# Kernel tuning notes

Measured on AMD Instinct MI355X. Metric: run time of the kernel, lower is better.

## Reference

```python
import jax, jax.numpy as jnp
import numpy as np
import math

N_HEADS = 16


def setup_inputs() -> dict:
    key = jax.random.key(0)
    ks = jax.random.split(key, 5)
    B, S, E = 2, 2048, 1024
    scale = 1.0 / math.sqrt(E)
    return {
        "x": jax.random.normal(ks[0], (B, S, E), dtype=jnp.float32),
        "w_in": jax.random.normal(ks[1], (3 * E, E), dtype=jnp.float32) * scale,
        "b_in": jax.random.normal(ks[2], (3 * E,), dtype=jnp.float32) * 0.01,
        "w_out": jax.random.normal(ks[3], (E, E), dtype=jnp.float32) * scale,
        "b_out": jax.random.normal(ks[4], (E,), dtype=jnp.float32) * 0.01,
    }


def reference(x, w_in, b_in, w_out, b_out):
    B, S, E = x.shape
    H = N_HEADS
    d = E // H
    # fused QKV projection: [B,S,3E]
    qkv = x @ w_in.T + b_in
    q, k, v = jnp.split(qkv, 3, axis=-1)
    # [B,S,E] -> [B,H,S,d]
    q = q.reshape(B, S, H, d).transpose(0, 2, 1, 3)
    k = k.reshape(B, S, H, d).transpose(0, 2, 1, 3)
    v = v.reshape(B, S, H, d).transpose(0, 2, 1, 3)
    # scores [B,H,S,S], scaled by 1/sqrt(d_head) (no causal mask: casual_mask=False)
    scores = jnp.einsum("bhqd,bhkd->bhqk", q, k) / jnp.sqrt(jnp.float32(d)).astype(x.dtype)
    w = jax.nn.softmax(scores, axis=-1)
    # attention output [B,H,S,d] -> [B,S,E]
    out = jnp.einsum("bhqk,bhkd->bhqd", w, v)
    out = out.transpose(0, 2, 1, 3).reshape(B, S, E)
    return out @ w_out.T + b_out
```

## Files before the change

kernel.cpp:

```cpp
#include <hip/hip_runtime.h>
#include <cstdint>


typedef __bf16 bf16x8 __attribute__((ext_vector_type(8)));
typedef short s16x4 __attribute__((ext_vector_type(4)));
typedef float f32x4 __attribute__((ext_vector_type(4)));

__device__ __forceinline__ unsigned short f32_to_bf16_rne(float f) {
    unsigned int u = __builtin_bit_cast(unsigned int, f);
    u += 0x7FFF + ((u >> 16) & 1);
    return (unsigned short)(u >> 16);
}

__device__ __forceinline__ unsigned int pack_bf16_trunc(float a, float b) {
    unsigned int ua = __builtin_bit_cast(unsigned int, a);
    unsigned int ub = __builtin_bit_cast(unsigned int, b);
    return __builtin_amdgcn_perm(ub, ua, 0x07060302u);
}

__device__ __forceinline__ void gload16(const void* g, void* l) {
    __builtin_amdgcn_global_load_lds(
        (const __attribute__((address_space(1))) unsigned int*)g,
        (__attribute__((address_space(3))) unsigned int*)l, 16, 0, 0);
}

__global__ void cvt_all(const float* __restrict__ x, const float* __restrict__ wi,
                        const float* __restrict__ wo, unsigned short* __restrict__ xb,
                        unsigned short* __restrict__ wib, unsigned short* __restrict__ wob) {
    int i = blockIdx.x * blockDim.x + threadIdx.x;
    const float* src; unsigned short* dst; int off;
    if (i < 1048576)            { src = x;  dst = xb;  off = i; }
    else if (i < 1048576 + 786432) { src = wi; dst = wib; off = i - 1048576; }
    else                        { src = wo; dst = wob; off = i - (1048576 + 786432); }
    float4 v = ((const float4*)src)[off];
    ushort4 o;
    o.x = f32_to_bf16_rne(v.x); o.y = f32_to_bf16_rne(v.y);
    o.z = f32_to_bf16_rne(v.z); o.w = f32_to_bf16_rne(v.w);
    ((ushort4*)dst)[off] = o;
}

__launch_bounds__(256)
__global__ void gemm_qkv(const unsigned short* __restrict__ X,
                         const unsigned short* __restrict__ W,
                         const float* __restrict__ bias,
                         unsigned short* __restrict__ Qp,
                         unsigned short* __restrict__ Kp,
                         unsigned short* __restrict__ Vt) {
    __shared__ __align__(16) unsigned short As[3][128 * 32];
    __shared__ __align__(16) unsigned short Bs[3][128 * 32];
    const int t = threadIdx.x;
    const int w = t >> 6, lane = t & 63, quad = lane >> 4, l16 = lane & 15;
    const int wm = (w >> 1) * 64, wn = (w & 1) * 64;
    const int lin = blockIdx.x;
    const int xcd = lin & 7, idx = lin >> 3;
    const int bx = (xcd & 1) * 12 + idx % 12;
    const int by = (xcd >> 1) * 8 + idx / 12;
    const int m0 = by * 128, n0 = bx * 128;

    const int c0 = t, c1 = t + 256;
    const int r0 = c0 >> 2, cc0 = (c0 & 3) * 8;
    const int r1 = c1 >> 2, cc1 = (c1 & 3) * 8;
#define QKV_STAGE(kt, buf)                                             \
    do {                                                               \
        gload16(&X[(m0 + r0) * 1024 + (kt) + cc0], &As[buf][c0 * 8]);  \
        gload16(&W[(n0 + r0) * 1024 + (kt) + cc0], &Bs[buf][c0 * 8]);  \
        gload16(&X[(m0 + r1) * 1024 + (kt) + cc1], &As[buf][c1 * 8]);  \
        gload16(&W[(n0 + r1) * 1024 + (kt) + cc1], &Bs[buf][c1 * 8]);  \
    } while (0)

    f32x4 acc[4][4] = {};

    QKV_STAGE(0, 0);
    QKV_STAGE(32, 1);

    int cur = 0, nxt = 1, nn = 2;
    for (int k = 0; k < 32; ++k) {
        if (k == 31) { asm volatile("s_waitcnt vmcnt(0)" ::: "memory"); }
        else         { asm volatile("s_waitcnt vmcnt(4)" ::: "memory"); }
        __builtin_amdgcn_s_barrier();
        asm volatile("" ::: "memory");
        if (k < 30) QKV_STAGE((k + 2) * 32, nn);
        const unsigned short* Ab = As[cur];
        const unsigned short* Bb = Bs[cur];
        bf16x8 af[4], bw[4];
#pragma unroll
        for (int mi = 0; mi < 4; ++mi)
            af[mi] = *(const bf16x8*)&Ab[(wm + mi * 16 + l16) * 32 + quad * 8];
#pragma unroll
        for (int ni = 0; ni < 4; ++ni)
            bw[ni] = *(const bf16x8*)&Bb[(wn + ni * 16 + l16) * 32 + quad * 8];
#pragma unroll
        for (int mi = 0; mi < 4; ++mi)
#pragma unroll
            for (int ni = 0; ni < 4; ++ni)
                acc[mi][ni] = __builtin_amdgcn_mfma_f32_16x16x32_bf16(af[mi], bw[ni], acc[mi][ni], 0, 0, 0);
        int tmp = cur; cur = nxt; nxt = nn; nn = tmp;
    }
#undef QKV_STAGE

    const float QSCALE = 0.125f * 1.44269504089f;
#pragma unroll
    for (int mi = 0; mi < 4; ++mi) {
#pragma unroll
        for (int ni = 0; ni < 4; ++ni) {
            int col = n0 + wn + ni * 16 + l16;
            float bv = bias[col];
            int which = col >> 10;
            int hc = col & 1023;
            int h = hc >> 6, d = hc & 63;
            int row0 = m0 + wm + mi * 16 + quad * 4;
            int b = row0 >> 11, s0 = row0 & 2047;
            int bh = b * 16 + h;
            if (which == 2) {
                ushort4 pk;
                pk.x = f32_to_bf16_rne(acc[mi][ni][0] + bv);
                pk.y = f32_to_bf16_rne(acc[mi][ni][1] + bv);
                pk.z = f32_to_bf16_rne(acc[mi][ni][2] + bv);
                pk.w = f32_to_bf16_rne(acc[mi][ni][3] + bv);
                *(ushort4*)&Vt[(bh * 64 + d) * 2048 + s0] = pk;
            } else if (which == 0) {
#pragma unroll
                for (int r = 0; r < 4; ++r)
                    Qp[(bh * 2048 + s0 + r) * 64 + d] =
                        f32_to_bf16_rne((acc[mi][ni][r] + bv) * QSCALE);
            } else {
#pragma unroll
                for (int r = 0; r < 4; ++r)
                    Kp[(bh * 2048 + s0 + r) * 64 + d] = f32_to_bf16_rne(acc[mi][ni][r] + bv);
            }
        }
    }
}

__launch_bounds__(256, 4)
__global__ void attn(const unsigned short* __restrict__ Qp, const unsigned short* __restrict__ Kp,
                     const unsigned short* __restrict__ Vt, unsigned short* __restrict__ A2) {
    __shared__ __align__(16) unsigned short Ks[2][64 * 64];
    __shared__ __align__(16) unsigned short Vs[2][64 * 64];
    const int t = threadIdx.x, lane = t & 63, quad = lane >> 4, l16 = lane & 15;
    const int w = t >> 6;
    const int wq = w & 1;
    const int wk = w >> 1;
    const int bh = blockIdx.x;
    const int qb = blockIdx.y;
    const unsigned short* Qh = Qp + bh * (2048 * 64);
    const unsigned short* Kh = Kp + bh * (2048 * 64);
    const unsigned short* Vh = Vt + bh * (64 * 2048);

    bf16x8 qf[2][2];
#pragma unroll
    for (int nq = 0; nq < 2; ++nq)
#pragma unroll
        for (int ks = 0; ks < 2; ++ks) {
            int row = qb * 64 + wq * 32 + nq * 16 + l16;
            qf[nq][ks] = *(const bf16x8*)&Qh[row * 64 + ks * 32 + quad * 8];
        }

    f32x4 o_acc[4][2] = {};
    float l_lane[2] = {0.f, 0.f};

#pragma unroll
    for (int i = 0; i < 2; ++i) {
        int c = t + 256 * i;
        int r = c >> 3, sc = ((c & 7) ^ (r & 7)) << 3;
        gload16(&Kh[r * 64 + sc], &Ks[0][c * 8]);
        gload16(&Vh[r * 2048 + sc], &Vs[0][c * 8]);
    }

    int cur = 0;
    for (int it = 0; it < 32; ++it) {
        __syncthreads();
        if (it != 31) {
            int ktn = (it + 1) * 64;
#pragma unroll
            for (int i = 0; i < 2; ++i) {
                int c = t + 256 * i;
                int r = c >> 3, sc = ((c & 7) ^ (r & 7)) << 3;
                gload16(&Kh[(ktn + r) * 64 + sc], &Ks[cur ^ 1][c * 8]);
                gload16(&Vh[r * 2048 + ktn + sc], &Vs[cur ^ 1][c * 8]);
            }
        }
        const unsigned short* Kc = Ks[cur];
        const unsigned short* Vc = Vs[cur];

        f32x4 s_acc[2][2] = {};
#pragma unroll
        for (int ks = 0; ks < 2; ++ks)
#pragma unroll
            for (int mi = 0; mi < 2; ++mi) {
                int row = wk * 32 + mi * 16 + l16;
                bf16x8 kf = *(const bf16x8*)&Kc[row * 64 +
                                                (((ks * 4 + quad) ^ (l16 & 7)) << 3)];
#pragma unroll
                for (int nq = 0; nq < 2; ++nq)
                    s_acc[mi][nq] = __builtin_amdgcn_mfma_f32_16x16x32_bf16(kf, qf[nq][ks], s_acc[mi][nq], 0, 0, 0);
            }

        s16x4 bq[2][2];
#pragma unroll
        for (int nq = 0; nq < 2; ++nq) {
            float rsum = 0.f;
#pragma unroll
            for (int mi = 0; mi < 2; ++mi) {
                float p0 = __builtin_amdgcn_exp2f(s_acc[mi][nq][0]);
                float p1 = __builtin_amdgcn_exp2f(s_acc[mi][nq][1]);
                float p2 = __builtin_amdgcn_exp2f(s_acc[mi][nq][2]);
                float p3 = __builtin_amdgcn_exp2f(s_acc[mi][nq][3]);
                rsum += (p0 + p1) + (p2 + p3);
                uint2 pk;
                pk.x = pack_bf16_trunc(p0, p1);
                pk.y = pack_bf16_trunc(p2, p3);
                bq[mi][nq] = __builtin_bit_cast(s16x4, pk);
            }
            l_lane[nq] += rsum;
        }

#pragma unroll
        for (int dm = 0; dm < 4; ++dm)
#pragma unroll
            for (int kt4 = 0; kt4 < 2; ++kt4) {
                int ch = (wk * 4 + kt4 * 2 + (quad >> 1)) ^ (l16 & 7);
                s16x4 av = __builtin_bit_cast(s16x4,
                    *(const uint2*)&Vc[(dm * 16 + l16) * 64 + (ch << 3) + (quad & 1) * 4]);
#pragma unroll
                for (int nq = 0; nq < 2; ++nq)
                    o_acc[dm][nq] = __builtin_amdgcn_mfma_f32_16x16x16bf16_1k(av, bq[kt4][nq], o_acc[dm][nq], 0, 0, 0);
            }
        cur ^= 1;
    }

    __syncthreads();
    float* fo = (float*)&Ks[0][0];
    float* fl = (float*)&Vs[0][0];
    if (wk == 1) {
#pragma unroll
        for (int nq = 0; nq < 2; ++nq) {
#pragma unroll
            for (int dm = 0; dm < 4; ++dm)
                *(f32x4*)&fo[(wq * 32 + nq * 16 + l16) * 64 + dm * 16 + quad * 4] = o_acc[dm][nq];
            fl[(wq * 2 + nq) * 64 + lane] = l_lane[nq];
        }
    }
    __syncthreads();
    if (wk == 0) {
        const int b = bh >> 4, h = bh & 15;
#pragma unroll
        for (int nq = 0; nq < 2; ++nq) {
#pragma unroll
            for (int dm = 0; dm < 4; ++dm)
                o_acc[dm][nq] += *(const f32x4*)&fo[(wq * 32 + nq * 16 + l16) * 64 + dm * 16 + quad * 4];
            float l = l_lane[nq] + fl[(wq * 2 + nq) * 64 + lane];
            l += __shfl_xor(l, 16);
            l += __shfl_xor(l, 32);
            float rl = 1.0f / l;
            int s = qb * 64 + wq * 32 + nq * 16 + l16;
            int tok = b * 2048 + s;
#pragma unroll
            for (int dm = 0; dm < 4; ++dm) {
                ushort4 o;
                o.x = f32_to_bf16_rne(o_acc[dm][nq][0] * rl);
                o.y = f32_to_bf16_rne(o_acc[dm][nq][1] * rl);
                o.z = f32_to_bf16_rne(o_acc[dm][nq][2] * rl);
                o.w = f32_to_bf16_rne(o_acc[dm][nq][3] * rl);
                *(ushort4*)&A2[tok * 1024 + h * 64 + dm * 16 + quad * 4] = o;
            }
        }
    }
}

__launch_bounds__(256)
__global__ void gemm_out_k(const unsigned short* __restrict__ A, const unsigned short* __restrict__ W,
                           const float* __restrict__ bias, float* __restrict__ out) {
    __shared__ __align__(16) unsigned short As[3][64 * 32];
    __shared__ __align__(16) unsigned short Bs[3][64 * 32];
    const int t = threadIdx.x;
    const int w = t >> 6, lane = t & 63, quad = lane >> 4, l16 = lane & 15;
    const int wm = (w >> 1) * 32, wn = (w & 1) * 32;
    const int lin = blockIdx.x;
    const int xcd = lin & 7, idx = lin >> 3;
    const int bx = (xcd & 1) * 8 + idx % 8;
    const int by = (xcd >> 1) * 16 + idx / 8;
    const int m0 = by * 64, n0 = bx * 64;

    const int r0 = t >> 2, cc0 = (t & 3) * 8;
#define OUT_STAGE(kt, buf)                                             \
    do {                                                               \
        gload16(&A[(m0 + r0) * 1024 + (kt) + cc0], &As[buf][t * 8]);   \
        gload16(&W[(n0 + r0) * 1024 + (kt) + cc0], &Bs[buf][t * 8]);   \
    } while (0)

    f32x4 acc[2][2] = {};

    OUT_STAGE(0, 0);
    OUT_STAGE(32, 1);

    int cur = 0, nxt = 1, nn = 2;
    for (int k = 0; k < 32; ++k) {
        if (k == 31) { asm volatile("s_waitcnt vmcnt(0)" ::: "memory"); }
        else         { asm volatile("s_waitcnt vmcnt(2)" ::: "memory"); }
        __builtin_amdgcn_s_barrier();
        asm volatile("" ::: "memory");
        if (k < 30) OUT_STAGE((k + 2) * 32, nn);
        const unsigned short* Ab = As[cur];
        const unsigned short* Bb = Bs[cur];
        bf16x8 af[2], bw[2];
#pragma unroll
        for (int mi = 0; mi < 2; ++mi)
            af[mi] = *(const bf16x8*)&Ab[(wm + mi * 16 + l16) * 32 + quad * 8];
#pragma unroll
        for (int ni = 0; ni < 2; ++ni)
            bw[ni] = *(const bf16x8*)&Bb[(wn + ni * 16 + l16) * 32 + quad * 8];
#pragma unroll
        for (int mi = 0; mi < 2; ++mi)
#pragma unroll
            for (int ni = 0; ni < 2; ++ni)
                acc[mi][ni] = __builtin_amdgcn_mfma_f32_16x16x32_bf16(af[mi], bw[ni], acc[mi][ni], 0, 0, 0);
        int tmp = cur; cur = nxt; nxt = nn; nn = tmp;
    }
#undef OUT_STAGE

#pragma unroll
    for (int mi = 0; mi < 2; ++mi)
#pragma unroll
        for (int ni = 0; ni < 2; ++ni) {
            int col = n0 + wn + ni * 16 + l16;
            float bv = bias[col];
#pragma unroll
            for (int r = 0; r < 4; ++r) {
                int row = m0 + wm + mi * 16 + quad * 4 + r;
                out[row * 1024 + col] = acc[mi][ni][r] + bv;
            }
        }
}

extern "C" void kernel_launch(void* const* d_in, const int* in_sizes, int n_in,
                              void* d_out, int out_size, void* d_ws, size_t ws_size,
                              hipStream_t stream) {
    const float* x     = (const float*)d_in[0];
    const float* w_in  = (const float*)d_in[1];
    const float* b_in  = (const float*)d_in[2];
    const float* w_out = (const float*)d_in[3];
    const float* b_out = (const float*)d_in[4];
    float* out = (float*)d_out;

    char* ws = (char*)d_ws;
    unsigned short* xb  = (unsigned short*)(ws);
    unsigned short* wib = (unsigned short*)(ws + 8388608);
    unsigned short* wob = (unsigned short*)(ws + 14680064);
    unsigned short* Qp  = (unsigned short*)(ws + 16777216);
    unsigned short* Kp  = (unsigned short*)(ws + 25165824);
    unsigned short* Vt  = (unsigned short*)(ws + 33554432);
    unsigned short* A2  = (unsigned short*)(ws + 41943040);

    cvt_all<<<8192, 256, 0, stream>>>(x, w_in, w_out, xb, wib, wob);
    gemm_qkv<<<768, 256, 0, stream>>>(xb, wib, b_in, Qp, Kp, Vt);
    attn<<<dim3(32, 32), 256, 0, stream>>>(Qp, Kp, Vt, A2);
    gemm_out_k<<<1024, 256, 0, stream>>>(A2, wob, b_out, out);
}
```

Before: 192.3 us.

## Halve attention query tile per block and compute softmax row sums with MFMA

Each attention block now handles 32 query rows instead of 64, and the grid is doubled along the query axis, so there are twice as many smaller blocks. The softmax denominator is now built by an extra MFMA that multiplies a ones matrix by the packed probabilities. This replaces the per-lane VALU adds and the cross-lane shuffles. The cost is that every K/V tile is loaded from global memory and LDS twice as often per query, and each wave issues fewer MFMAs per LDS load.

```diff
diff --git a/kernel.cpp b/kernel.cpp
--- a/kernel.cpp
+++ b/kernel.cpp
@@ -147,17 +147,16 @@
     const unsigned short* Kh = Kp + bh * (2048 * 64);
     const unsigned short* Vh = Vt + bh * (64 * 2048);
 
-    bf16x8 qf[2][2];
-#pragma unroll
-    for (int nq = 0; nq < 2; ++nq)
-#pragma unroll
-        for (int ks = 0; ks < 2; ++ks) {
-            int row = qb * 64 + wq * 32 + nq * 16 + l16;
-            qf[nq][ks] = *(const bf16x8*)&Qh[row * 64 + ks * 32 + quad * 8];
-        }
-
-    f32x4 o_acc[4][2] = {};
-    float l_lane[2] = {0.f, 0.f};
+    bf16x8 qf[2];
+#pragma unroll
+    for (int ks = 0; ks < 2; ++ks) {
+        int row = qb * 32 + wq * 16 + l16;
+        qf[ks] = *(const bf16x8*)&Qh[row * 64 + ks * 32 + quad * 8];
+    }
+
+    f32x4 o_acc[4] = {};
+    f32x4 acc_l = {};
+    const s16x4 av_ones = {(short)0x3F80, (short)0x3F80, (short)0x3F80, (short)0x3F80};
 
 #pragma unroll
     for (int i = 0; i < 2; ++i) {
@@ -183,7 +182,7 @@
         const unsigned short* Kc = Ks[cur];
         const unsigned short* Vc = Vs[cur];
 
-        f32x4 s_acc[2][2] = {};
+        f32x4 s_acc[2] = {};
 #pragma unroll
         for (int ks = 0; ks < 2; ++ks)
 #pragma unroll
@@ -191,29 +190,24 @@
                 int row = wk * 32 + mi * 16 + l16;
                 bf16x8 kf = *(const bf16x8*)&Kc[row * 64 +
                                                 (((ks * 4 + quad) ^ (l16 & 7)) << 3)];
-#pragma unroll
-                for (int nq = 0; nq < 2; ++nq)
-                    s_acc[mi][nq] = __builtin_amdgcn_mfma_f32_16x16x32_bf16(kf, qf[nq][ks], s_acc[mi][nq], 0, 0, 0);
-            }
-
-        s16x4 bq[2][2];
-#pragma unroll
-        for (int nq = 0; nq < 2; ++nq) {
-            float rsum = 0.f;
-#pragma unroll
-            for (int mi = 0; mi < 2; ++mi) {
-                float p0 = __builtin_amdgcn_exp2f(s_acc[mi][nq][0]);
-                float p1 = __builtin_amdgcn_exp2f(s_acc[mi][nq][1]);
-                float p2 = __builtin_amdgcn_exp2f(s_acc[mi][nq][2]);
-                float p3 = __builtin_amdgcn_exp2f(s_acc[mi][nq][3]);
-                rsum += (p0 + p1) + (p2 + p3);
-                uint2 pk;
-                pk.x = pack_bf16_trunc(p0, p1);
-                pk.y = pack_bf16_trunc(p2, p3);
-                bq[mi][nq] = __builtin_bit_cast(s16x4, pk);
-            }
-            l_lane[nq] += rsum;
-        }
+                s_acc[mi] = __builtin_amdgcn_mfma_f32_16x16x32_bf16(kf, qf[ks], s_acc[mi], 0, 0, 0);
+            }
+
+        s16x4 bq[2];
+#pragma unroll
+        for (int mi = 0; mi < 2; ++mi) {
+            float p0 = __builtin_amdgcn_exp2f(s_acc[mi][0]);
+            float p1 = __builtin_amdgcn_exp2f(s_acc[mi][1]);
+            float p2 = __builtin_amdgcn_exp2f(s_acc[mi][2]);
+            float p3 = __builtin_amdgcn_exp2f(s_acc[mi][3]);
+            uint2 pk;
+            pk.x = pack_bf16_trunc(p0, p1);
+            pk.y = pack_bf16_trunc(p2, p3);
+            bq[mi] = __builtin_bit_cast(s16x4, pk);
+        }
+
+        acc_l = __builtin_amdgcn_mfma_f32_16x16x16bf16_1k(av_ones, bq[0], acc_l, 0, 0, 0);
+        acc_l = __builtin_amdgcn_mfma_f32_16x16x16bf16_1k(av_ones, bq[1], acc_l, 0, 0, 0);
 
 #pragma unroll
         for (int dm = 0; dm < 4; ++dm)
@@ -222,9 +216,7 @@
                 int ch = (wk * 4 + kt4 * 2 + (quad >> 1)) ^ (l16 & 7);
                 s16x4 av = __builtin_bit_cast(s16x4,
                     *(const uint2*)&Vc[(dm * 16 + l16) * 64 + (ch << 3) + (quad & 1) * 4]);
-#pragma unroll
-                for (int nq = 0; nq < 2; ++nq)
-                    o_acc[dm][nq] = __builtin_amdgcn_mfma_f32_16x16x16bf16_1k(av, bq[kt4][nq], o_acc[dm][nq], 0, 0, 0);
+                o_acc[dm] = __builtin_amdgcn_mfma_f32_16x16x16bf16_1k(av, bq[kt4], o_acc[dm], 0, 0, 0);
             }
         cur ^= 1;
     }
@@ -234,36 +226,28 @@
     float* fl = (float*)&Vs[0][0];
     if (wk == 1) {
 #pragma unroll
-        for (int nq = 0; nq < 2; ++nq) {
-#pragma unroll
-            for (int dm = 0; dm < 4; ++dm)
-                *(f32x4*)&fo[(wq * 32 + nq * 16 + l16) * 64 + dm * 16 + quad * 4] = o_acc[dm][nq];
-            fl[(wq * 2 + nq) * 64 + lane] = l_lane[nq];
-        }
+        for (int dm = 0; dm < 4; ++dm)
+            *(f32x4*)&fo[(wq * 16 + l16) * 64 + dm * 16 + quad * 4] = o_acc[dm];
+        fl[wq * 64 + lane] = acc_l[0];
     }
     __syncthreads();
     if (wk == 0) {
         const int b = bh >> 4, h = bh & 15;
 #pragma unroll
-        for (int nq = 0; nq < 2; ++nq) {
-#pragma unroll
-            for (int dm = 0; dm < 4; ++dm)
-                o_acc[dm][nq] += *(const f32x4*)&fo[(wq * 32 + nq * 16 + l16) * 64 + dm * 16 + quad * 4];
-            float l = l_lane[nq] + fl[(wq * 2 + nq) * 64 + lane];
-            l += __shfl_xor(l, 16);
-            l += __shfl_xor(l, 32);
-            float rl = 1.0f / l;
-            int s = qb * 64 + wq * 32 + nq * 16 + l16;
-            int tok = b * 2048 + s;
-#pragma unroll
-            for (int dm = 0; dm < 4; ++dm) {
-                ushort4 o;
-                o.x = f32_to_bf16_rne(o_acc[dm][nq][0] * rl);
-                o.y = f32_to_bf16_rne(o_acc[dm][nq][1] * rl);
-                o.z = f32_to_bf16_rne(o_acc[dm][nq][2] * rl);
-                o.w = f32_to_bf16_rne(o_acc[dm][nq][3] * rl);
-                *(ushort4*)&A2[tok * 1024 + h * 64 + dm * 16 + quad * 4] = o;
-            }
+        for (int dm = 0; dm < 4; ++dm)
+            o_acc[dm] += *(const f32x4*)&fo[(wq * 16 + l16) * 64 + dm * 16 + quad * 4];
+        float l = acc_l[0] + fl[wq * 64 + lane];
+        float rl = 1.0f / l;
+        int s = qb * 32 + wq * 16 + l16;
+        int tok = b * 2048 + s;
+#pragma unroll
+        for (int dm = 0; dm < 4; ++dm) {
+            ushort4 o;
+            o.x = f32_to_bf16_rne(o_acc[dm][0] * rl);
+            o.y = f32_to_bf16_rne(o_acc[dm][1] * rl);
+            o.z = f32_to_bf16_rne(o_acc[dm][2] * rl);
+            o.w = f32_to_bf16_rne(o_acc[dm][3] * rl);
+            *(ushort4*)&A2[tok * 1024 + h * 64 + dm * 16 + quad * 4] = o;
         }
     }
 }
@@ -354,6 +338,6 @@
 
     cvt_all<<<8192, 256, 0, stream>>>(x, w_in, w_out, xb, wib, wob);
     gemm_qkv<<<768, 256, 0, stream>>>(xb, wib, b_in, Qp, Kp, Vt);
-    attn<<<dim3(32, 32), 256, 0, stream>>>(Qp, Kp, Vt, A2);
+    attn<<<dim3(32, 64), 256, 0, stream>>>(Qp, Kp, Vt, A2);
     gemm_out_k<<<1024, 256, 0, stream>>>(A2, wob, b_out, out);
 }
```

Measured after the change: 203.3 us. 5.7% more time.

## Triple-buffer attention K/V loads and compute softmax row sums via MFMA

Applied to the files above, without the earlier changes.

The attention kernel moves from a double-buffered to a triple-buffered K/V LDS pipeline. It prefetches two tiles ahead and uses explicit vmcnt waits with a bare barrier in place of __syncthreads, so global loads stay in flight across iterations. Softmax denominators are now accumulated with an extra MFMA against a ones vector instead of scalar adds plus cross-lane shuffles, which also uses the bf16-rounded probabilities. s_setprio is raised around the MFMA section. The cost is 50% more LDS per block, which may reduce occupancy at 4 blocks per CU.

```diff
diff --git a/kernel.cpp b/kernel.cpp
--- a/kernel.cpp
+++ b/kernel.cpp
@@ -135,8 +135,8 @@
 __launch_bounds__(256, 4)
 __global__ void attn(const unsigned short* __restrict__ Qp, const unsigned short* __restrict__ Kp,
                      const unsigned short* __restrict__ Vt, unsigned short* __restrict__ A2) {
-    __shared__ __align__(16) unsigned short Ks[2][64 * 64];
-    __shared__ __align__(16) unsigned short Vs[2][64 * 64];
+    __shared__ __align__(16) unsigned short Ks[3][64 * 64];
+    __shared__ __align__(16) unsigned short Vs[3][64 * 64];
     const int t = threadIdx.x, lane = t & 63, quad = lane >> 4, l16 = lane & 15;
     const int w = t >> 6;
     const int wq = w & 1;
@@ -157,29 +157,30 @@
         }
 
     f32x4 o_acc[4][2] = {};
-    float l_lane[2] = {0.f, 0.f};
-
-#pragma unroll
-    for (int i = 0; i < 2; ++i) {
-        int c = t + 256 * i;
-        int r = c >> 3, sc = ((c & 7) ^ (r & 7)) << 3;
-        gload16(&Kh[r * 64 + sc], &Ks[0][c * 8]);
-        gload16(&Vh[r * 2048 + sc], &Vs[0][c * 8]);
-    }
-
-    int cur = 0;
+    f32x4 acc_l[2] = {};
+    const s16x4 av_ones = {(short)0x3F80, (short)0x3F80, (short)0x3F80, (short)0x3F80};
+
+#define ATTN_STAGE(ktn, buf)                                               \
+    do {                                                                   \
+        _Pragma("unroll")                                                  \
+        for (int i = 0; i < 2; ++i) {                                      \
+            int c = t + 256 * i;                                           \
+            int r = c >> 3, sc = ((c & 7) ^ (r & 7)) << 3;                 \
+            gload16(&Kh[((ktn) + r) * 64 + sc], &Ks[buf][c * 8]);          \
+            gload16(&Vh[r * 2048 + (ktn) + sc], &Vs[buf][c * 8]);          \
+        }                                                                  \
+    } while (0)
+
+    ATTN_STAGE(0, 0);
+    ATTN_STAGE(64, 1);
+
+    int cur = 0, nxt = 1, nn = 2;
     for (int it = 0; it < 32; ++it) {
-        __syncthreads();
-        if (it != 31) {
-            int ktn = (it + 1) * 64;
-#pragma unroll
-            for (int i = 0; i < 2; ++i) {
-                int c = t + 256 * i;
-                int r = c >> 3, sc = ((c & 7) ^ (r & 7)) << 3;
-                gload16(&Kh[(ktn + r) * 64 + sc], &Ks[cur ^ 1][c * 8]);
-                gload16(&Vh[r * 2048 + ktn + sc], &Vs[cur ^ 1][c * 8]);
-            }
-        }
+        if (it == 31) { asm volatile("s_waitcnt vmcnt(0)" ::: "memory"); }
+        else          { asm volatile("s_waitcnt vmcnt(4)" ::: "memory"); }
+        __builtin_amdgcn_s_barrier();
+        asm volatile("" ::: "memory");
+        if (it < 30) ATTN_STAGE((it + 2) * 64, nn);
         const unsigned short* Kc = Ks[cur];
         const unsigned short* Vc = Vs[cur];
 
@@ -198,21 +199,24 @@
 
         s16x4 bq[2][2];
 #pragma unroll
-        for (int nq = 0; nq < 2; ++nq) {
-            float rsum = 0.f;
+        for (int nq = 0; nq < 2; ++nq)
 #pragma unroll
             for (int mi = 0; mi < 2; ++mi) {
                 float p0 = __builtin_amdgcn_exp2f(s_acc[mi][nq][0]);
                 float p1 = __builtin_amdgcn_exp2f(s_acc[mi][nq][1]);
                 float p2 = __builtin_amdgcn_exp2f(s_acc[mi][nq][2]);
                 float p3 = __builtin_amdgcn_exp2f(s_acc[mi][nq][3]);
-                rsum += (p0 + p1) + (p2 + p3);
                 uint2 pk;
                 pk.x = pack_bf16_trunc(p0, p1);
                 pk.y = pack_bf16_trunc(p2, p3);
                 bq[mi][nq] = __builtin_bit_cast(s16x4, pk);
             }
-            l_lane[nq] += rsum;
+
+        __builtin_amdgcn_s_setprio(1);
+#pragma unroll
+        for (int nq = 0; nq < 2; ++nq) {
+            acc_l[nq] = __builtin_amdgcn_mfma_f32_16x16x16bf16_1k(av_ones, bq[0][nq], acc_l[nq], 0, 0, 0);
+            acc_l[nq] = __builtin_amdgcn_mfma_f32_16x16x16bf16_1k(av_ones, bq[1][nq], acc_l[nq], 0, 0, 0);
         }
 
 #pragma unroll
@@ -226,8 +230,10 @@
                 for (int nq = 0; nq < 2; ++nq)
                     o_acc[dm][nq] = __builtin_amdgcn_mfma_f32_16x16x16bf16_1k(av, bq[kt4][nq], o_acc[dm][nq], 0, 0, 0);
             }
-        cur ^= 1;
-    }
+        __builtin_amdgcn_s_setprio(0);
+        int tmp = cur; cur = nxt; nxt = nn; nn = tmp;
+    }
+#undef ATTN_STAGE
 
     __syncthreads();
     float* fo = (float*)&Ks[0][0];
@@ -238,7 +244,7 @@
 #pragma unroll
             for (int dm = 0; dm < 4; ++dm)
                 *(f32x4*)&fo[(wq * 32 + nq * 16 + l16) * 64 + dm * 16 + quad * 4] = o_acc[dm][nq];
-            fl[(wq * 2 + nq) * 64 + lane] = l_lane[nq];
+            fl[(wq * 2 + nq) * 64 + lane] = acc_l[nq][0];
         }
     }
     __syncthreads();
@@ -249,9 +255,7 @@
 #pragma unroll
             for (int dm = 0; dm < 4; ++dm)
                 o_acc[dm][nq] += *(const f32x4*)&fo[(wq * 32 + nq * 16 + l16) * 64 + dm * 16 + quad * 4];
-            float l = l_lane[nq] + fl[(wq * 2 + nq) * 64 + lane];
-            l += __shfl_xor(l, 16);
-            l += __shfl_xor(l, 32);
+            float l = acc_l[nq][0] + fl[(wq * 2 + nq) * 64 + lane];
             float rl = 1.0f / l;
             int s = qb * 64 + wq * 32 + nq * 16 + l16;
             int tok = b * 2048 + s;
```

Result: slower. 206.2 us (+7.2%).
